# Optimization experiments

Measured on AMD Instinct MI355X. Metric: run time of the kernel, lower is better.

## Reference

```python
import jax, jax.numpy as jnp
import numpy as np

B, T, F, H = 256, 32, 128, 128
NUM_FILTERS, KH, KW, NUM_CLASSES = 64, 2, 2, 2
FLAT = NUM_FILTERS * (T - KH + 1) * (2 * F - KW + 1)  # 64*31*255 = 505920


def setup_inputs() -> dict:
    key = jax.random.key(0)
    ks = jax.random.split(key, 12)
    inp = {
        "X_nume": jax.random.normal(ks[0], (B, T, F), jnp.float32),
        "att_W": jax.random.uniform(ks[1], (F, H), jnp.float32),
        "att_U": jax.random.uniform(ks[2], (F, H), jnp.float32),
        "att_V": jax.random.uniform(ks[3], (H, 1), jnp.float32),
        "conv_w": jax.random.normal(ks[4], (NUM_FILTERS, 1, KH, KW), jnp.float32) * 0.5,
        "conv_b": jax.random.normal(ks[5], (NUM_FILTERS,), jnp.float32) * 0.1,
        "w1": jax.random.normal(ks[6], (FLAT, 256), jnp.float32) * (1.0 / np.sqrt(FLAT)),
        "b1": jnp.zeros((256,), jnp.float32),
        "w2": jax.random.normal(ks[7], (256, 32), jnp.float32) * (1.0 / np.sqrt(256)),
        "b2": jnp.zeros((32,), jnp.float32),
        "w3": jax.random.normal(ks[8], (32, NUM_CLASSES), jnp.float32) * (1.0 / np.sqrt(32)),
        "b3": jnp.zeros((NUM_CLASSES,), jnp.float32),
    }
    return inp


def reference(X_nume, att_W, att_U, att_V, conv_w, conv_b, w1, b1, w2, b2, w3, b3):
    X = X_nume  # [B, T, F]
    # --- additive attention, fully batched (replaces O(T^2) python loops) ---
    xw = jnp.einsum("btf,fh->bth", X, att_W)  # query proj [B,T,H]
    xu = jnp.einsum("btf,fh->bth", X, att_U)  # key proj   [B,T,H]
    # e[b,i,j] = V^T tanh(x_i W + x_j U)
    scores = jnp.squeeze(jnp.tanh(xw[:, :, None, :] + xu[:, None, :, :]) @ att_V, -1)  # [B,T,T]
    alpha = jax.nn.softmax(scores, axis=-1)  # softmax over j (includes diagonal)
    # context excludes j == i (original skips j == index AFTER softmax)
    mask = 1.0 - jnp.eye(T, dtype=X.dtype)
    c = jnp.einsum("bij,bjf->bif", alpha * mask, X)  # [B,T,F]
    feat = jnp.concatenate([X, c], axis=-1)  # [B,T,2F]
    # --- conv ---
    conv_in = feat[:, None, :, :]  # [B,1,T,2F]
    conv = jax.lax.conv_general_dilated(
        conv_in, conv_w, window_strides=(1, 1), padding="VALID",
        dimension_numbers=("NCHW", "OIHW", "NCHW"))
    conv = jax.nn.relu(conv + conv_b[None, :, None, None])  # [B,64,T-1,2F-1]
    # --- MLP head ---
    flat = conv.reshape(conv.shape[0], -1)
    h = jax.nn.relu(flat @ w1 + b1)
    h = jax.nn.relu(h @ w2 + b2)
    return h @ w3 + b3
```

## Files before the change

kernel.cpp:

```cpp
#include <hip/hip_runtime.h>
#include <hip/hip_bf16.h>

#define B_ 256
#define T_ 32
#define F_ 128
#define H_ 128
#define NF 64
#define OH 31
#define OW 255
#define POS_TOTAL (OH*OW)
#define N1 256
#define KT 248
#define NPB 4
#define NSTEPS (NPB*8)

typedef __attribute__((ext_vector_type(8))) short bf16x8;
typedef __attribute__((ext_vector_type(4))) float f32x4;

__device__ __forceinline__ unsigned short f2bf_rne(float f) {
    unsigned int u = __float_as_uint(f);
    u += 0x7FFFu + ((u >> 16) & 1u);
    return (unsigned short)(u >> 16);
}

__global__ __launch_bounds__(256) void k_attn(
    const float* __restrict__ X, const float* __restrict__ W,
    const float* __restrict__ U, const float* __restrict__ V,
    float* __restrict__ featL)
{
    __shared__ float Xs[T_][F_];
    __shared__ float xw[T_][H_];
    __shared__ float xu[T_][H_];
    __shared__ float sc[T_][T_];
    __shared__ float Vs[H_];

    const int b = blockIdx.x;
    const int t = threadIdx.x;
    const float* Xb = X + (size_t)b * T_ * F_;

    for (int idx = t; idx < T_*F_; idx += 256) ((float*)Xs)[idx] = Xb[idx];
    if (t < H_) Vs[t] = V[t];
    __syncthreads();

    {
        const int h = t & 127, half = t >> 7;
        float aw[16], au[16];
        #pragma unroll
        for (int r = 0; r < 16; r++) { aw[r] = 0.f; au[r] = 0.f; }
        for (int f = 0; f < F_; f++) {
            const float wv = W[f*H_ + h];
            const float uv = U[f*H_ + h];
            #pragma unroll
            for (int r = 0; r < 16; r++) {
                const float xv = Xs[half*16 + r][f];
                aw[r] += xv * wv;
                au[r] += xv * uv;
            }
        }
        #pragma unroll
        for (int r = 0; r < 16; r++) {
            xw[half*16 + r][h] = aw[r];
            xu[half*16 + r][h] = au[r];
        }
    }
    __syncthreads();

    {
        const int i = t >> 3;
        const int j0 = (t & 7) * 4;
        float s0 = 0.f, s1 = 0.f, s2 = 0.f, s3 = 0.f;
        for (int h = 0; h < H_; h++) {
            const float xwv = xw[i][h];
            const float vv  = Vs[h];
            s0 += tanhf(xwv + xu[j0+0][h]) * vv;
            s1 += tanhf(xwv + xu[j0+1][h]) * vv;
            s2 += tanhf(xwv + xu[j0+2][h]) * vv;
            s3 += tanhf(xwv + xu[j0+3][h]) * vv;
        }
        sc[i][j0+0] = s0; sc[i][j0+1] = s1; sc[i][j0+2] = s2; sc[i][j0+3] = s3;
    }
    __syncthreads();

    if (t < T_) {
        float m = -1e30f;
        #pragma unroll
        for (int j = 0; j < T_; j++) m = fmaxf(m, sc[t][j]);
        float sum = 0.f;
        #pragma unroll
        for (int j = 0; j < T_; j++) sum += expf(sc[t][j] - m);
        const float inv = 1.f / sum;
        #pragma unroll
        for (int j = 0; j < T_; j++) {
            const float a = expf(sc[t][j] - m) * inv;
            sc[t][j] = (j == t) ? 0.f : a;
        }
    }
    __syncthreads();

    for (int idx = t; idx < T_*F_; idx += 256) {
        const int row = idx >> 7, f = idx & 127;
        float acc = 0.f;
        #pragma unroll
        for (int j = 0; j < T_; j++) acc += sc[row][j] * Xs[j][f];
        float* fr = featL + (size_t)b*8192 + row*256;
        fr[f]       = Xs[row][f];
        fr[128 + f] = acc;
    }
}

__global__ __launch_bounds__(256) void k_tr(
    const float* __restrict__ src, float* __restrict__ dst)
{
    __shared__ float tile[32][33];
    const int rc0 = blockIdx.x * 32;
    const int b0  = blockIdx.y * 32;
    const int tx = threadIdx.x & 31;
    const int ty = threadIdx.x >> 5;
    #pragma unroll
    for (int r = 0; r < 32; r += 8)
        tile[ty + r][tx] = src[(size_t)(b0 + ty + r)*8192 + rc0 + tx];
    __syncthreads();
    #pragma unroll
    for (int r = 0; r < 32; r += 8)
        dst[(size_t)(rc0 + ty + r)*256 + b0 + tx] = tile[tx][ty + r];
}

__global__ __launch_bounds__(512, 2) void k_gemm1(
    const float* __restrict__ featT, const float* __restrict__ cw,
    const float* __restrict__ cb, const float* __restrict__ w1,
    float* __restrict__ partial)
{
    __shared__ unsigned short As[2][256*64];
    __shared__ unsigned short Ws[2][256*64];
    __shared__ float cwL[256];
    __shared__ float cbL[64];

    const int t  = threadIdx.x;
    const int kt = blockIdx.x;

    if (t < 256) cwL[t] = cw[t];
    if (t < 64)  cbL[t] = cb[t];

    const int rn  = t & 255;
    const int fq2 = t >> 8;
    const int rsw = rn & 7;

    const int lane = t & 63, wid = t >> 6;
    const int wm = (wid >> 2) * 128;
    const int wn = (wid & 3) * 64;
    const int fr = lane & 15, fq = lane >> 4;

    f32x4 acc[8][4];
    #pragma unroll
    for (int i = 0; i < 8; i++)
        #pragma unroll
        for (int j = 0; j < 4; j++)
            acc[i][j] = (f32x4){0.f, 0.f, 0.f, 0.f};

    float patch[4][8];
    float wvv[4][8];

    const int pb0 = kt * NPB;

#define PATCH_LOADS(PB)                                                        \
    {                                                                          \
        const int pbase_ = (PB) * 8;                                           \
        _Pragma("unroll")                                                      \
        for (int pi = 0; pi < 8; pi++) {                                       \
            int pos_ = pbase_ + pi;                                            \
            if (pos_ > POS_TOTAL-1) pos_ = POS_TOTAL-1;                        \
            const int y_ = pos_ / 255;                                         \
            const int x_ = pos_ - y_*255;                                      \
            const float* fp_ = featT + ((size_t)(y_*256 + x_))*256 + rn;       \
            patch[0][pi] = fp_[0];                                             \
            patch[1][pi] = fp_[256];                                           \
            patch[2][pi] = fp_[65536];                                         \
            patch[3][pi] = fp_[65536 + 256];                                   \
        }                                                                      \
    }

#define W_LOADS(SG)                                                            \
    {                                                                          \
        const int pbase_ = (pb0 + ((SG) >> 3)) * 8;                            \
        const int fg_ = (SG) & 7;                                              \
        _Pragma("unroll")                                                      \
        for (int fl = 0; fl < 4; fl++) {                                       \
            const int f_ = fg_*8 + fq2*4 + fl;                                 \
            _Pragma("unroll")                                                  \
            for (int pi = 0; pi < 8; pi++) {                                   \
                int pos_ = pbase_ + pi;                                        \
                if (pos_ > POS_TOTAL-1) pos_ = POS_TOTAL-1;                    \
                wvv[fl][pi] = w1[(size_t)(f_*POS_TOTAL + pos_)*N1 + rn];       \
            }                                                                  \
        }                                                                      \
    }

#define STAGE_WRITE(BUF, SG)                                                   \
    {                                                                          \
        const int pbase_ = (pb0 + ((SG) >> 3)) * 8;                            \
        const int fg_ = (SG) & 7;                                              \
        _Pragma("unroll")                                                      \
        for (int fl = 0; fl < 4; fl++) {                                       \
            const int f_ = fg_*8 + fq2*4 + fl;                                 \
            const float4 cc_ = *(const float4*)&cwL[f_*4];                     \
            const float cbv_ = cbL[f_];                                        \
            unsigned int apk_[4], wpk_[4];                                     \
            _Pragma("unroll")                                                  \
            for (int pi = 0; pi < 8; pi++) {                                   \
                float v_ = patch[0][pi]*cc_.x + patch[1][pi]*cc_.y             \
                         + patch[2][pi]*cc_.z + patch[3][pi]*cc_.w + cbv_;     \
                v_ = (pbase_ + pi < POS_TOTAL) ? fmaxf(v_, 0.f) : 0.f;         \
                const unsigned short ab_ = f2bf_rne(v_);                       \
                const unsigned short wb_ = f2bf_rne(wvv[fl][pi]);              \
                if (pi & 1) { apk_[pi>>1] |= (unsigned int)ab_ << 16;          \
                              wpk_[pi>>1] |= (unsigned int)wb_ << 16; }        \
                else        { apk_[pi>>1]  = ab_; wpk_[pi>>1]  = wb_; }        \
            }                                                                  \
            const int blk_ = (fq2*4 + fl) ^ rsw;                               \
            *(uint4*)&As[BUF][rn*64 + blk_*8] = *(uint4*)&apk_[0];             \
            *(uint4*)&Ws[BUF][rn*64 + blk_*8] = *(uint4*)&wpk_[0];             \
        }                                                                      \
    }

#define DO_MFMA(BUF)                                                           \
    {                                                                          \
        _Pragma("unroll")                                                      \
        for (int c = 0; c < 2; c++) {                                          \
            const int swz_ = ((c*4 + fq) ^ (fr & 7)) * 8;                      \
            bf16x8 af_[8], bf_[4];                                             \
            _Pragma("unroll")                                                  \
            for (int mg = 0; mg < 8; mg++)                                     \
                af_[mg] = *(const bf16x8*)&As[BUF][(wm + mg*16 + fr)*64 + swz_];\
            _Pragma("unroll")                                                  \
            for (int ng = 0; ng < 4; ng++)                                     \
                bf_[ng] = *(const bf16x8*)&Ws[BUF][(wn + ng*16 + fr)*64 + swz_];\
            _Pragma("unroll")                                                  \
            for (int mg = 0; mg < 8; mg++)                                     \
                _Pragma("unroll")                                              \
                for (int ng = 0; ng < 4; ng++)                                 \
                    acc[mg][ng] = __builtin_amdgcn_mfma_f32_16x16x32_bf16(     \
                        af_[mg], bf_[ng], acc[mg][ng], 0, 0, 0);               \
        }                                                                      \
    }

    PATCH_LOADS(pb0);
    W_LOADS(0);
    __syncthreads();
    STAGE_WRITE(0, 0);
    __syncthreads();

    #pragma unroll 1
    for (int S = 0; S < NSTEPS; S++) {
        const int cur = S & 1;
        if (S + 1 < NSTEPS) {
            if (((S + 1) & 7) == 0) PATCH_LOADS(pb0 + ((S + 1) >> 3));
            W_LOADS(S + 1);
        }
        DO_MFMA(cur);
        if (S + 1 < NSTEPS) STAGE_WRITE(cur ^ 1, S + 1);
        __syncthreads();
    }

    float* pp = partial + (size_t)kt * (256*256);
    #pragma unroll
    for (int mg = 0; mg < 8; mg++)
        #pragma unroll
        for (int ng = 0; ng < 4; ng++) {
            const int col = wn + ng*16 + fr;
            #pragma unroll
            for (int j = 0; j < 4; j++) {
                const int row = wm + mg*16 + fq*4 + j;
                pp[(size_t)row*256 + col] = acc[mg][ng][j];
            }
        }
#undef PATCH_LOADS
#undef W_LOADS
#undef STAGE_WRITE
#undef DO_MFMA
}

__global__ __launch_bounds__(256) void k_head(
    const float* __restrict__ partial, int KT_,
    const float* __restrict__ b1, const float* __restrict__ w2,
    const float* __restrict__ b2, const float* __restrict__ w3,
    const float* __restrict__ b3, float* __restrict__ out)
{
    __shared__ float h1s[256];
    __shared__ float h2s[32];
    const int b = blockIdx.x, t = threadIdx.x;

    float s = b1[t];
    for (int kt = 0; kt < KT_; kt++)
        s += partial[(size_t)kt*(256*N1) + (size_t)b*N1 + t];
    h1s[t] = fmaxf(s, 0.f);
    __syncthreads();

    if (t < 32) {
        float s2 = b2[t];
        for (int i = 0; i < 256; i++) s2 += h1s[i] * w2[i*32 + t];
        h2s[t] = fmaxf(s2, 0.f);
    }
    __syncthreads();

    if (t < 2) {
        float s3 = b3[t];
        #pragma unroll
        for (int i = 0; i < 32; i++) s3 += h2s[i] * w3[i*2 + t];
        out[b*2 + t] = s3;
    }
}

extern "C" void kernel_launch(void* const* d_in, const int* in_sizes, int n_in,
                              void* d_out, int out_size, void* d_ws, size_t ws_size,
                              hipStream_t stream) {
    const float* X    = (const float*)d_in[0];
    const float* attW = (const float*)d_in[1];
    const float* attU = (const float*)d_in[2];
    const float* attV = (const float*)d_in[3];
    const float* cw   = (const float*)d_in[4];
    const float* cb   = (const float*)d_in[5];
    const float* w1   = (const float*)d_in[6];
    const float* b1   = (const float*)d_in[7];
    const float* w2   = (const float*)d_in[8];
    const float* b2   = (const float*)d_in[9];
    const float* w3   = (const float*)d_in[10];
    const float* b3   = (const float*)d_in[11];
    float* out = (float*)d_out;

    float* featL   = (float*)d_ws;
    float* featT   = (float*)((char*)d_ws + (8u<<20));
    float* partial = (float*)((char*)d_ws + (16u<<20));

    k_attn <<<dim3(B_),       dim3(256), 0, stream>>>(X, attW, attU, attV, featL);
    k_tr   <<<dim3(256, 8),   dim3(256), 0, stream>>>(featL, featT);
    k_gemm1<<<dim3(KT),       dim3(512), 0, stream>>>(featT, cw, cb, w1, partial);
    k_head <<<dim3(B_),       dim3(256), 0, stream>>>(partial, KT, b1, w2, b2, w3, b3, out);
}
```

Baseline: 324.5 us.

## Halve GEMM1 K-step to 32 with blocked LDS layout for higher occupancy

Measured after the change: 324.3 us. No clear change (-0.1%).

```diff
diff --git a/kernel.cpp b/kernel.cpp
--- a/kernel.cpp
+++ b/kernel.cpp
@@ -11,8 +11,7 @@
 #define POS_TOTAL (OH*OW)
 #define N1 256
 #define KT 248
-#define NPB 4
-#define NSTEPS (NPB*8)
+#define NSTEPS 64
 
 typedef __attribute__((ext_vector_type(8))) short bf16x8;
 typedef __attribute__((ext_vector_type(4))) float f32x4;
@@ -130,8 +129,8 @@
     const float* __restrict__ cb, const float* __restrict__ w1,
     float* __restrict__ partial)
 {
-    __shared__ unsigned short As[2][256*64];
-    __shared__ unsigned short Ws[2][256*64];
+    __shared__ unsigned short As[2*4*256*8];
+    __shared__ unsigned short Ws[2*4*256*8];
     __shared__ float cwL[256];
     __shared__ float cbL[64];
 
@@ -143,7 +142,6 @@
 
     const int rn  = t & 255;
     const int fq2 = t >> 8;
-    const int rsw = rn & 7;
 
     const int lane = t & 63, wid = t >> 6;
     const int wm = (wid >> 2) * 128;
@@ -158,9 +156,9 @@
             acc[i][j] = (f32x4){0.f, 0.f, 0.f, 0.f};
 
     float patch[4][8];
-    float wvv[4][8];
-
-    const int pb0 = kt * NPB;
+    float wvv[2][8];
+
+    const int pb0 = kt * 4;
 
 #define PATCH_LOADS(PB)                                                        \
     {                                                                          \
@@ -181,27 +179,27 @@
 
 #define W_LOADS(SG)                                                            \
     {                                                                          \
-        const int pbase_ = (pb0 + ((SG) >> 3)) * 8;                            \
-        const int fg_ = (SG) & 7;                                              \
-        _Pragma("unroll")                                                      \
-        for (int fl = 0; fl < 4; fl++) {                                       \
-            const int f_ = fg_*8 + fq2*4 + fl;                                 \
+        const int fg_ = (SG) & 15;                                             \
+        const int pbase_ = (pb0 + ((SG) >> 4)) * 8;                            \
+        _Pragma("unroll")                                                      \
+        for (int j = 0; j < 2; j++) {                                          \
+            const int f_ = fg_*4 + fq2*2 + j;                                  \
             _Pragma("unroll")                                                  \
             for (int pi = 0; pi < 8; pi++) {                                   \
                 int pos_ = pbase_ + pi;                                        \
                 if (pos_ > POS_TOTAL-1) pos_ = POS_TOTAL-1;                    \
-                wvv[fl][pi] = w1[(size_t)(f_*POS_TOTAL + pos_)*N1 + rn];       \
+                wvv[j][pi] = w1[(size_t)(f_*POS_TOTAL + pos_)*N1 + rn];        \
             }                                                                  \
         }                                                                      \
     }
 
 #define STAGE_WRITE(BUF, SG)                                                   \
     {                                                                          \
-        const int pbase_ = (pb0 + ((SG) >> 3)) * 8;                            \
-        const int fg_ = (SG) & 7;                                              \
-        _Pragma("unroll")                                                      \
-        for (int fl = 0; fl < 4; fl++) {                                       \
-            const int f_ = fg_*8 + fq2*4 + fl;                                 \
+        const int fg_ = (SG) & 15;                                             \
+        const int pbase_ = (pb0 + ((SG) >> 4)) * 8;                            \
+        _Pragma("unroll")                                                      \
+        for (int j = 0; j < 2; j++) {                                          \
+            const int f_ = fg_*4 + fq2*2 + j;                                  \
             const float4 cc_ = *(const float4*)&cwL[f_*4];                     \
             const float cbv_ = cbL[f_];                                        \
             unsigned int apk_[4], wpk_[4];                                     \
@@ -211,36 +209,32 @@
                          + patch[2][pi]*cc_.z + patch[3][pi]*cc_.w + cbv_;     \
                 v_ = (pbase_ + pi < POS_TOTAL) ? fmaxf(v_, 0.f) : 0.f;         \
                 const unsigned short ab_ = f2bf_rne(v_);                       \
-                const unsigned short wb_ = f2bf_rne(wvv[fl][pi]);              \
+                const unsigned short wb_ = f2bf_rne(wvv[j][pi]);               \
                 if (pi & 1) { apk_[pi>>1] |= (unsigned int)ab_ << 16;          \
                               wpk_[pi>>1] |= (unsigned int)wb_ << 16; }        \
                 else        { apk_[pi>>1]  = ab_; wpk_[pi>>1]  = wb_; }        \
             }                                                                  \
-            const int blk_ = (fq2*4 + fl) ^ rsw;                               \
-            *(uint4*)&As[BUF][rn*64 + blk_*8] = *(uint4*)&apk_[0];             \
-            *(uint4*)&Ws[BUF][rn*64 + blk_*8] = *(uint4*)&wpk_[0];             \
+            const int blk_ = fq2*2 + j;                                        \
+            *(uint4*)&As[(((BUF)*4 + blk_)*256 + rn)*8] = *(uint4*)&apk_[0];   \
+            *(uint4*)&Ws[(((BUF)*4 + blk_)*256 + rn)*8] = *(uint4*)&wpk_[0];   \
         }                                                                      \
     }
 
 #define DO_MFMA(BUF)                                                           \
     {                                                                          \
-        _Pragma("unroll")                                                      \
-        for (int c = 0; c < 2; c++) {                                          \
-            const int swz_ = ((c*4 + fq) ^ (fr & 7)) * 8;                      \
-            bf16x8 af_[8], bf_[4];                                             \
-            _Pragma("unroll")                                                  \
-            for (int mg = 0; mg < 8; mg++)                                     \
-                af_[mg] = *(const bf16x8*)&As[BUF][(wm + mg*16 + fr)*64 + swz_];\
+        bf16x8 af_[8], bf_[4];                                                 \
+        _Pragma("unroll")                                                      \
+        for (int mg = 0; mg < 8; mg++)                                         \
+            af_[mg] = *(const bf16x8*)&As[(((BUF)*4 + fq)*256 + wm+mg*16+fr)*8];\
+        _Pragma("unroll")                                                      \
+        for (int ng = 0; ng < 4; ng++)                                         \
+            bf_[ng] = *(const bf16x8*)&Ws[(((BUF)*4 + fq)*256 + wn+ng*16+fr)*8];\
+        _Pragma("unroll")                                                      \
+        for (int mg = 0; mg < 8; mg++)                                         \
             _Pragma("unroll")                                                  \
             for (int ng = 0; ng < 4; ng++)                                     \
-                bf_[ng] = *(const bf16x8*)&Ws[BUF][(wn + ng*16 + fr)*64 + swz_];\
-            _Pragma("unroll")                                                  \
-            for (int mg = 0; mg < 8; mg++)                                     \
-                _Pragma("unroll")                                              \
-                for (int ng = 0; ng < 4; ng++)                                 \
-                    acc[mg][ng] = __builtin_amdgcn_mfma_f32_16x16x32_bf16(     \
-                        af_[mg], bf_[ng], acc[mg][ng], 0, 0, 0);               \
-        }                                                                      \
+                acc[mg][ng] = __builtin_amdgcn_mfma_f32_16x16x32_bf16(         \
+                    af_[mg], bf_[ng], acc[mg][ng], 0, 0, 0);                   \
     }
 
     PATCH_LOADS(pb0);
@@ -253,7 +247,7 @@
     for (int S = 0; S < NSTEPS; S++) {
         const int cur = S & 1;
         if (S + 1 < NSTEPS) {
-            if (((S + 1) & 7) == 0) PATCH_LOADS(pb0 + ((S + 1) >> 3));
+            if (((S + 1) & 15) == 0) PATCH_LOADS(pb0 + ((S + 1) >> 4));
             W_LOADS(S + 1);
         }
         DO_MFMA(cur);
```
